# Performance work log

Hardware: AMD Instinct MI355X
Metric: run time of the kernel (lower is better)

## Reference

```python
import jax, jax.numpy as jnp
import numpy as np

N_NODES = 100000
N_EDGES = 1600000
NFEAT, NHID, NCLASS = 128, 64, 40


def setup_inputs() -> dict:
    key = jax.random.key(0)
    k_x, k_e, k_w1, k_b1, k_w2, k_b2 = jax.random.split(key, 6)
    x = jax.random.normal(k_x, (N_NODES, NFEAT), dtype=jnp.float32)
    edge_index = jax.random.randint(k_e, (2, N_EDGES), 0, N_NODES, dtype=jnp.int32)
    # Linear params (torch Linear stores weight as [out, in])
    W1 = jax.random.normal(k_w1, (NHID, NFEAT), dtype=jnp.float32) * 0.05
    b1 = jax.random.normal(k_b1, (NHID,), dtype=jnp.float32) * 0.05
    W2 = jax.random.normal(k_w2, (NCLASS, NHID), dtype=jnp.float32) * 0.05
    b2 = jax.random.normal(k_b2, (NCLASS,), dtype=jnp.float32) * 0.05
    return {"x": x, "W1": W1, "b1": b1, "W2": W2, "b2": b2, "edge_index": edge_index}


def _gcn_layer(x, src, dst, W, b):
    """One GraphConvolution: linear, then degree-normalized gather-scale-scatter-add."""
    n = x.shape[0]
    h = x @ W.T + b  # [N, out]
    # degree computed over row (= src), as in the torch message(); self-loops guarantee deg >= 1
    deg = jax.ops.segment_sum(jnp.ones(src.shape[0], dtype=h.dtype), src, num_segments=n)
    dinv = jax.lax.rsqrt(deg)
    norm = dinv[src] * dinv[dst]  # [E]
    msg = norm[:, None] * h[src]  # gather + scale, [E, out]
    return jax.ops.segment_sum(msg, dst, num_segments=n)  # scatter-add into targets


def reference(x, W1, b1, W2, b2, edge_index):
    n = x.shape[0]
    loops = jnp.arange(n, dtype=edge_index.dtype)
    src = jnp.concatenate([edge_index[0], loops])  # add_self_loops
    dst = jnp.concatenate([edge_index[1], loops])
    h = jax.nn.relu(_gcn_layer(x, src, dst, W1, b1))
    # dropout is identity in eval mode (single-partition: owned_nodes == all nodes,
    # so the distributed halo-exchange / feature-replacement block is a no-op)
    out = _gcn_layer(h, src, dst, W2, b2)
    return jax.nn.log_softmax(out, axis=1)
```

## Files before the change

kernel.cpp:

```cpp
#include <hip/hip_runtime.h>
#include <hip/hip_fp16.h>

#define N_NODES 100000
#define N_EDGES 1600000
#define NFEAT 128
#define NHID 64
#define NCLASS 40
#define SCAN_B 256
#define NTOT (N_NODES + 1)
#define PEMAX (N_EDGES + 16 * N_NODES)

#define BPG 8192
#define NGROUPS 13
#define NCHUNKS 32
#define CHUNK_E (N_EDGES / NCHUNKS)
#define HBINS (NGROUPS * BPG)

#define XROWS 80
#define RPT 20

__global__ __launch_bounds__(256) void hist_kernel(const int* __restrict__ src,
                                                   const int* __restrict__ dst,
                                                   int* __restrict__ deg_src,
                                                   int* __restrict__ hc,
                                                   int* __restrict__ rank) {
    __shared__ int hs[BPG], hd[BPG];
    int g = blockIdx.x, c = blockIdx.y;
    int lo = g * BPG;
    for (int i = threadIdx.x; i < BPG; i += 256) { hs[i] = 0; hd[i] = 0; }
    __syncthreads();
    const int4* s4 = (const int4*)(src + (size_t)c * CHUNK_E);
    const int4* d4 = (const int4*)(dst + (size_t)c * CHUNK_E);
    int n4 = CHUNK_E / 4;
    for (int i = threadIdx.x; i < n4; i += 256) {
        int4 s = s4[i], d = d4[i];
        if ((unsigned)(s.x - lo) < BPG) atomicAdd(&hs[s.x - lo], 1);
        if ((unsigned)(s.y - lo) < BPG) atomicAdd(&hs[s.y - lo], 1);
        if ((unsigned)(s.z - lo) < BPG) atomicAdd(&hs[s.z - lo], 1);
        if ((unsigned)(s.w - lo) < BPG) atomicAdd(&hs[s.w - lo], 1);
        int eb = c * CHUNK_E + 4 * i;
        if ((unsigned)(d.x - lo) < BPG) rank[eb + 0] = atomicAdd(&hd[d.x - lo], 1);
        if ((unsigned)(d.y - lo) < BPG) rank[eb + 1] = atomicAdd(&hd[d.y - lo], 1);
        if ((unsigned)(d.z - lo) < BPG) rank[eb + 2] = atomicAdd(&hd[d.z - lo], 1);
        if ((unsigned)(d.w - lo) < BPG) rank[eb + 3] = atomicAdd(&hd[d.w - lo], 1);
    }
    __syncthreads();
    for (int i = threadIdx.x; i < BPG; i += 256) {
        int v = hs[i];
        if (v) atomicAdd(&deg_src[lo + i], v);
        hc[(size_t)c * HBINS + lo + i] = hd[i];
    }
}

__global__ void dinv_kernel(const int* __restrict__ deg, float* __restrict__ dinv) {
    int i = blockIdx.x * blockDim.x + threadIdx.x;
    if (i < N_NODES) dinv[i] = rsqrtf((float)(deg[i] + 1));
}

__global__ void colsum_kernel(const int* __restrict__ hc, int* __restrict__ pcnt) {
    int b = blockIdx.x * 256 + threadIdx.x;
    if (b >= NTOT) return;
    if (b == N_NODES) { pcnt[b] = 0; return; }
    int s = 0;
    #pragma unroll 8
    for (int c = 0; c < NCHUNKS; ++c) s += hc[(size_t)c * HBINS + b];
    pcnt[b] = (s + 15) & ~15;
}

__global__ void scan1_kernel(const int* __restrict__ cnt, int* __restrict__ partial,
                             int* __restrict__ bsums) {
    __shared__ int tmp[SCAN_B];
    int gid = blockIdx.x * SCAN_B + threadIdx.x;
    int v = (gid < NTOT) ? cnt[gid] : 0;
    tmp[threadIdx.x] = v;
    __syncthreads();
    for (int off = 1; off < SCAN_B; off <<= 1) {
        int t = (threadIdx.x >= off) ? tmp[threadIdx.x - off] : 0;
        __syncthreads();
        tmp[threadIdx.x] += t;
        __syncthreads();
    }
    if (gid < NTOT) partial[gid] = tmp[threadIdx.x] - v;
    if (threadIdx.x == SCAN_B - 1) bsums[blockIdx.x] = tmp[threadIdx.x];
}

__global__ void scan2_kernel(int* __restrict__ bsums, int nb) {
    __shared__ int tmp[512];
    int v = (threadIdx.x < nb) ? bsums[threadIdx.x] : 0;
    tmp[threadIdx.x] = v;
    __syncthreads();
    for (int off = 1; off < 512; off <<= 1) {
        int t = (threadIdx.x >= off) ? tmp[threadIdx.x - off] : 0;
        __syncthreads();
        tmp[threadIdx.x] += t;
        __syncthreads();
    }
    if (threadIdx.x < nb) bsums[threadIdx.x] = tmp[threadIdx.x] - v;
}

__global__ void scan3_kernel(const int* __restrict__ partial, const int* __restrict__ bsums,
                             int* __restrict__ offs) {
    int gid = blockIdx.x * 256 + threadIdx.x;
    if (gid < NTOT) offs[gid] = partial[gid] + bsums[gid >> 8];
}

__global__ void colbase_kernel(const int* __restrict__ hc, const int* __restrict__ offs,
                               int* __restrict__ base) {
    int b = blockIdx.x * 256 + threadIdx.x;
    if (b >= N_NODES) return;
    int r = offs[b];
    #pragma unroll 8
    for (int c = 0; c < NCHUNKS; ++c) {
        base[(size_t)c * HBINS + b] = r;
        r += hc[(size_t)c * HBINS + b];
    }
}

__global__ __launch_bounds__(256) void fill3_kernel(const int* __restrict__ src,
                                                    const int* __restrict__ dst,
                                                    const float* __restrict__ dinv,
                                                    const int* __restrict__ base,
                                                    const int* __restrict__ rank,
                                                    int2* __restrict__ edges) {
    int e = blockIdx.x * 256 + threadIdx.x;
    if (e >= N_EDGES) return;
    int s = src[e], d = dst[e];
    int c = e / CHUNK_E;
    int pos = base[(size_t)c * HBINS + d] + rank[e];
    edges[pos] = make_int2(s, __float_as_int(dinv[s] * dinv[d]));
}

__global__ __launch_bounds__(256) void gemm1_kernel(const float* __restrict__ x,
                                                    const float* __restrict__ W1,
                                                    const float* __restrict__ b1,
                                                    __half* __restrict__ h) {
    __shared__ float xs[XROWS * NFEAT];
    __shared__ float wq[(NFEAT / 4) * NHID * 4];
    int tid = threadIdx.x;
    const float4* w4 = (const float4*)W1;
    for (int j = tid; j < NFEAT * NHID / 4; j += 256) {
        int col = j >> 5, k4 = j & 31;
        int rcol = (col + k4) & 63;
        *(float4*)&wq[(k4 * 64 + rcol) * 4] = w4[j];
    }
    int row0 = blockIdx.x * XROWS;
    const float4* xg = (const float4*)(x + (size_t)row0 * NFEAT);
    float4* xs4 = (float4*)xs;
    #pragma unroll 4
    for (int j = tid; j < XROWS * NFEAT / 4; j += 256) xs4[j] = xg[j];
    __syncthreads();

    int col = tid & 63;
    int rg  = tid >> 6;
    const float* xrow = xs + rg * RPT * NFEAT;
    float acc[RPT];
    #pragma unroll
    for (int r = 0; r < RPT; ++r) acc[r] = 0.f;

    #pragma unroll 2
    for (int k4 = 0; k4 < NFEAT / 4; ++k4) {
        int rcol = (col + k4) & 63;
        float4 w = *(const float4*)&wq[(k4 * 64 + rcol) * 4];
        #pragma unroll
        for (int r = 0; r < RPT; ++r) {
            float4 a = *(const float4*)&xrow[r * NFEAT + k4 * 4];
            acc[r] += a.x * w.x + a.y * w.y + a.z * w.z + a.w * w.w;
        }
    }
    float bb = b1[col];
    #pragma unroll
    for (int r = 0; r < RPT; ++r)
        h[(size_t)(row0 + rg * RPT + r) * NHID + col] = __float2half(acc[r] + bb);
}

__global__ __launch_bounds__(256) void agg1_kernel(const int* __restrict__ offs,
                                                   const float* __restrict__ dinv,
                                                   const int2* __restrict__ edges,
                                                   const __half* __restrict__ h,
                                                   __half* __restrict__ z) {
    int wid = (blockIdx.x * 256 + threadIdx.x) >> 6;
    if (wid >= N_NODES) return;
    int lane = threadIdx.x & 63;
    int hw = lane >> 5;
    int fl = lane & 31;
    int start = offs[wid];
    int myn = (offs[wid + 1] - start) >> 1;
    const int2* eb = edges + start + hw * myn;
    float ax = 0.f, ay = 0.f;
    for (int j = 0; j < myn; j += 8) {
        int2 e0 = eb[j],     e1 = eb[j + 1], e2 = eb[j + 2], e3 = eb[j + 3];
        int2 e4 = eb[j + 4], e5 = eb[j + 5], e6 = eb[j + 6], e7 = eb[j + 7];
        float2 f0 = __half22float2(*(const __half2*)(h + ((size_t)e0.x << 6) + 2 * fl));
        float2 f1 = __half22float2(*(const __half2*)(h + ((size_t)e1.x << 6) + 2 * fl));
        float2 f2 = __half22float2(*(const __half2*)(h + ((size_t)e2.x << 6) + 2 * fl));
        float2 f3 = __half22float2(*(const __half2*)(h + ((size_t)e3.x << 6) + 2 * fl));
        float2 f4 = __half22float2(*(const __half2*)(h + ((size_t)e4.x << 6) + 2 * fl));
        float2 f5 = __half22float2(*(const __half2*)(h + ((size_t)e5.x << 6) + 2 * fl));
        float2 f6 = __half22float2(*(const __half2*)(h + ((size_t)e6.x << 6) + 2 * fl));
        float2 f7 = __half22float2(*(const __half2*)(h + ((size_t)e7.x << 6) + 2 * fl));
        float w0 = __int_as_float(e0.y), w1 = __int_as_float(e1.y);
        float w2 = __int_as_float(e2.y), w3 = __int_as_float(e3.y);
        float w4 = __int_as_float(e4.y), w5 = __int_as_float(e5.y);
        float w6 = __int_as_float(e6.y), w7 = __int_as_float(e7.y);
        ax += w0 * f0.x + w1 * f1.x + w2 * f2.x + w3 * f3.x
            + w4 * f4.x + w5 * f5.x + w6 * f6.x + w7 * f7.x;
        ay += w0 * f0.y + w1 * f1.y + w2 * f2.y + w3 * f3.y
            + w4 * f4.y + w5 * f5.y + w6 * f6.y + w7 * f7.y;
    }
    ax += __shfl_xor(ax, 32);
    ay += __shfl_xor(ay, 32);
    if (hw == 0) {
        float di = dinv[wid];
        float2 f = __half22float2(*(const __half2*)(h + ((size_t)wid << 6) + 2 * fl));
        ax += di * di * f.x;
        ay += di * di * f.y;
        *(__half2*)(z + ((size_t)wid << 6) + 2 * fl) =
            __floats2half2_rn(fmaxf(ax, 0.f), fmaxf(ay, 0.f));
    }
}

__global__ __launch_bounds__(256) void agg2f_kernel(const int* __restrict__ offs,
                                                    const float* __restrict__ dinv,
                                                    const int2* __restrict__ edges,
                                                    const __half* __restrict__ z,
                                                    const float* __restrict__ W2,
                                                    const float* __restrict__ b2,
                                                    float* __restrict__ out) {
    __shared__ float W2l[NHID * NCLASS];
    __shared__ float b2l[NCLASS];
    __shared__ float zs[4 * NHID];
    for (int idx = threadIdx.x; idx < NCLASS * NHID; idx += 256) {
        int c = idx / NHID, k = idx % NHID;
        W2l[k * NCLASS + c] = W2[idx];
    }
    if (threadIdx.x < NCLASS) b2l[threadIdx.x] = b2[threadIdx.x];
    __syncthreads();

    int wid = (blockIdx.x * 256 + threadIdx.x) >> 6;
    if (wid >= N_NODES) return;
    int lane = threadIdx.x & 63;
    int wv = threadIdx.x >> 6;
    int hw = lane >> 5;
    int fl = lane & 31;
    int start = offs[wid];
    int myn = (offs[wid + 1] - start) >> 1;
    const int2* eb = edges + start + hw * myn;
    float ax = 0.f, ay = 0.f, wsum = 0.f;
    for (int j = 0; j < myn; j += 8) {
        int2 e0 = eb[j],     e1 = eb[j + 1], e2 = eb[j + 2], e3 = eb[j + 3];
        int2 e4 = eb[j + 4], e5 = eb[j + 5], e6 = eb[j + 6], e7 = eb[j + 7];
        float2 f0 = __half22float2(*(const __half2*)(z + ((size_t)e0.x << 6) + 2 * fl));
        float2 f1 = __half22float2(*(const __half2*)(z + ((size_t)e1.x << 6) + 2 * fl));
        float2 f2 = __half22float2(*(const __half2*)(z + ((size_t)e2.x << 6) + 2 * fl));
        float2 f3 = __half22float2(*(const __half2*)(z + ((size_t)e3.x << 6) + 2 * fl));
        float2 f4 = __half22float2(*(const __half2*)(z + ((size_t)e4.x << 6) + 2 * fl));
        float2 f5 = __half22float2(*(const __half2*)(z + ((size_t)e5.x << 6) + 2 * fl));
        float2 f6 = __half22float2(*(const __half2*)(z + ((size_t)e6.x << 6) + 2 * fl));
        float2 f7 = __half22float2(*(const __half2*)(z + ((size_t)e7.x << 6) + 2 * fl));
        float w0 = __int_as_float(e0.y), w1 = __int_as_float(e1.y);
        float w2 = __int_as_float(e2.y), w3 = __int_as_float(e3.y);
        float w4 = __int_as_float(e4.y), w5 = __int_as_float(e5.y);
        float w6 = __int_as_float(e6.y), w7 = __int_as_float(e7.y);
        ax += w0 * f0.x + w1 * f1.x + w2 * f2.x + w3 * f3.x
            + w4 * f4.x + w5 * f5.x + w6 * f6.x + w7 * f7.x;
        ay += w0 * f0.y + w1 * f1.y + w2 * f2.y + w3 * f3.y
            + w4 * f4.y + w5 * f5.y + w6 * f6.y + w7 * f7.y;
        wsum += w0 + w1 + w2 + w3 + w4 + w5 + w6 + w7;
    }
    ax += __shfl_xor(ax, 32);
    ay += __shfl_xor(ay, 32);
    wsum += __shfl_xor(wsum, 32);
    float di = dinv[wid];
    float dsq = di * di;
    float2 fz = __half22float2(*(const __half2*)(z + ((size_t)wid << 6) + 2 * fl));
    ax += dsq * fz.x;
    ay += dsq * fz.y;
    wsum += dsq;
    if (hw == 0) *(float2*)&zs[wv * NHID + 2 * fl] = make_float2(ax, ay);
    int c = lane;
    float acc = 0.f;
    if (c < NCLASS) {
        const float* zw = &zs[wv * NHID];
        #pragma unroll 8
        for (int k = 0; k < NHID; ++k) acc += zw[k] * W2l[k * NCLASS + c];
        acc += wsum * b2l[c];
    }
    float m = (c < NCLASS) ? acc : -INFINITY;
    #pragma unroll
    for (int o = 32; o > 0; o >>= 1) m = fmaxf(m, __shfl_xor(m, o));
    float ex = (c < NCLASS) ? __expf(acc - m) : 0.f;
    float s = ex;
    #pragma unroll
    for (int o = 32; o > 0; o >>= 1) s += __shfl_xor(s, o);
    if (c < NCLASS) out[(size_t)wid * NCLASS + c] = acc - m - logf(s);
}

extern "C" void kernel_launch(void* const* d_in, const int* in_sizes, int n_in,
                              void* d_out, int out_size, void* d_ws, size_t ws_size,
                              hipStream_t stream) {
    const float* x  = (const float*)d_in[0];
    const float* W1 = (const float*)d_in[1];
    const float* b1 = (const float*)d_in[2];
    const float* W2 = (const float*)d_in[3];
    const float* b2 = (const float*)d_in[4];
    const int*   ei = (const int*)d_in[5];
    const int* src = ei;
    const int* dst = ei + N_EDGES;
    float* out = (float*)d_out;

    char* ws = (char*)d_ws;
    int*    deg_src = (int*)ws;    ws += 400128;
    int*    pcnt    = (int*)ws;    ws += 400128;
    int*    offs    = (int*)ws;    ws += 400128;
    int*    partial = (int*)ws;    ws += 400128;
    int*    bsums   = (int*)ws;    ws += 2048;
    float*  dinv    = (float*)ws;  ws += 400128;
    int*    hc      = (int*)ws;    ws += (size_t)NCHUNKS * HBINS * sizeof(int);
    int*    base    = (int*)ws;    ws += (size_t)NCHUNKS * HBINS * sizeof(int);
    int*    rank    = (int*)ws;    ws += (size_t)N_EDGES * sizeof(int);
    int2*   edges   = (int2*)ws;   ws += (size_t)PEMAX * sizeof(int2);
    __half* h       = (__half*)ws; ws += (size_t)N_NODES * NHID * sizeof(__half);
    __half* z       = (__half*)ws; ws += (size_t)N_NODES * NHID * sizeof(__half);

    hipMemsetAsync(deg_src, 0, (size_t)N_NODES * sizeof(int), stream);
    hipMemsetAsync(edges, 0, (size_t)PEMAX * sizeof(int2), stream);

    dim3 hgrid(NGROUPS, NCHUNKS);
    hist_kernel<<<hgrid, 256, 0, stream>>>(src, dst, deg_src, hc, rank);
    dinv_kernel<<<(N_NODES + 255) / 256, 256, 0, stream>>>(deg_src, dinv);
    colsum_kernel<<<(NTOT + 255) / 256, 256, 0, stream>>>(hc, pcnt);

    int nsb = (NTOT + SCAN_B - 1) / SCAN_B;
    scan1_kernel<<<nsb, SCAN_B, 0, stream>>>(pcnt, partial, bsums);
    scan2_kernel<<<1, 512, 0, stream>>>(bsums, nsb);
    scan3_kernel<<<(NTOT + 255) / 256, 256, 0, stream>>>(partial, bsums, offs);
    colbase_kernel<<<(N_NODES + 255) / 256, 256, 0, stream>>>(hc, offs, base);

    fill3_kernel<<<(N_EDGES + 255) / 256, 256, 0, stream>>>(src, dst, dinv, base, rank, edges);

    gemm1_kernel<<<N_NODES / XROWS, 256, 0, stream>>>(x, W1, b1, h);

    int nwblk = (N_NODES * 64 + 255) / 256;
    agg1_kernel<<<nwblk, 256, 0, stream>>>(offs, dinv, edges, h, z);
    agg2f_kernel<<<nwblk, 256, 0, stream>>>(offs, dinv, edges, z, W2, b2, out);
}
```

Measured before the change: 294.9 us.

## Apply W2 before second aggregation so gather uses 40-wide features

Splits the fused aggregate-then-project kernel into a separate GEMM (z·W2ᵀ+b2 stored as fp16 in a 64-stride buffer) followed by an aggregation over the 40 projected columns with log_softmax. This reorders linear projection and aggregation so the gather only reads 40 of 64 columns per edge and drops the per-node matvec and weight-sum from the aggregation. It adds an extra kernel launch, an extra intermediate buffer round trip, and extra fp16 rounding of the projected values. Gathered row stride stays 128 bytes, so cache-line traffic per edge may not shrink much.

```diff
diff --git a/kernel.cpp b/kernel.cpp
--- a/kernel.cpp
+++ b/kernel.cpp
@@ -219,80 +219,85 @@
     }
 }
 
-__global__ __launch_bounds__(256) void agg2f_kernel(const int* __restrict__ offs,
-                                                    const float* __restrict__ dinv,
-                                                    const int2* __restrict__ edges,
-                                                    const __half* __restrict__ z,
+__global__ __launch_bounds__(256) void gemm2_kernel(const __half* __restrict__ z,
                                                     const float* __restrict__ W2,
                                                     const float* __restrict__ b2,
-                                                    float* __restrict__ out) {
-    __shared__ float W2l[NHID * NCLASS];
-    __shared__ float b2l[NCLASS];
-    __shared__ float zs[4 * NHID];
+                                                    __half* __restrict__ h2p) {
+    __shared__ float Wl[NHID * NCLASS];
     for (int idx = threadIdx.x; idx < NCLASS * NHID; idx += 256) {
         int c = idx / NHID, k = idx % NHID;
-        W2l[k * NCLASS + c] = W2[idx];
-    }
-    if (threadIdx.x < NCLASS) b2l[threadIdx.x] = b2[threadIdx.x];
-    __syncthreads();
-
+        Wl[k * NCLASS + c] = W2[idx];
+    }
+    __syncthreads();
+    int i = blockIdx.x * 256 + threadIdx.x;
+    if (i >= N_NODES * NCLASS) return;
+    int row = i / NCLASS, col = i - row * NCLASS;
+    const __half2* a = (const __half2*)(z + (size_t)row * NHID);
+    float acc = b2[col];
+    #pragma unroll 8
+    for (int k2 = 0; k2 < NHID / 2; ++k2) {
+        float2 f = __half22float2(a[k2]);
+        acc += f.x * Wl[(2 * k2) * NCLASS + col] + f.y * Wl[(2 * k2 + 1) * NCLASS + col];
+    }
+    h2p[((size_t)row << 6) + col] = __float2half(acc);
+}
+
+__global__ __launch_bounds__(256) void agg2_kernel(const int* __restrict__ offs,
+                                                   const float* __restrict__ dinv,
+                                                   const int2* __restrict__ edges,
+                                                   const __half* __restrict__ h2p,
+                                                   float* __restrict__ out) {
     int wid = (blockIdx.x * 256 + threadIdx.x) >> 6;
     if (wid >= N_NODES) return;
     int lane = threadIdx.x & 63;
-    int wv = threadIdx.x >> 6;
     int hw = lane >> 5;
     int fl = lane & 31;
+    bool act = fl < NCLASS / 2;
     int start = offs[wid];
     int myn = (offs[wid + 1] - start) >> 1;
     const int2* eb = edges + start + hw * myn;
-    float ax = 0.f, ay = 0.f, wsum = 0.f;
-    for (int j = 0; j < myn; j += 8) {
-        int2 e0 = eb[j],     e1 = eb[j + 1], e2 = eb[j + 2], e3 = eb[j + 3];
-        int2 e4 = eb[j + 4], e5 = eb[j + 5], e6 = eb[j + 6], e7 = eb[j + 7];
-        float2 f0 = __half22float2(*(const __half2*)(z + ((size_t)e0.x << 6) + 2 * fl));
-        float2 f1 = __half22float2(*(const __half2*)(z + ((size_t)e1.x << 6) + 2 * fl));
-        float2 f2 = __half22float2(*(const __half2*)(z + ((size_t)e2.x << 6) + 2 * fl));
-        float2 f3 = __half22float2(*(const __half2*)(z + ((size_t)e3.x << 6) + 2 * fl));
-        float2 f4 = __half22float2(*(const __half2*)(z + ((size_t)e4.x << 6) + 2 * fl));
-        float2 f5 = __half22float2(*(const __half2*)(z + ((size_t)e5.x << 6) + 2 * fl));
-        float2 f6 = __half22float2(*(const __half2*)(z + ((size_t)e6.x << 6) + 2 * fl));
-        float2 f7 = __half22float2(*(const __half2*)(z + ((size_t)e7.x << 6) + 2 * fl));
-        float w0 = __int_as_float(e0.y), w1 = __int_as_float(e1.y);
-        float w2 = __int_as_float(e2.y), w3 = __int_as_float(e3.y);
-        float w4 = __int_as_float(e4.y), w5 = __int_as_float(e5.y);
-        float w6 = __int_as_float(e6.y), w7 = __int_as_float(e7.y);
-        ax += w0 * f0.x + w1 * f1.x + w2 * f2.x + w3 * f3.x
-            + w4 * f4.x + w5 * f5.x + w6 * f6.x + w7 * f7.x;
-        ay += w0 * f0.y + w1 * f1.y + w2 * f2.y + w3 * f3.y
-            + w4 * f4.y + w5 * f5.y + w6 * f6.y + w7 * f7.y;
-        wsum += w0 + w1 + w2 + w3 + w4 + w5 + w6 + w7;
+    float ax = 0.f, ay = 0.f;
+    if (act) {
+        for (int j = 0; j < myn; j += 8) {
+            int2 e0 = eb[j],     e1 = eb[j + 1], e2 = eb[j + 2], e3 = eb[j + 3];
+            int2 e4 = eb[j + 4], e5 = eb[j + 5], e6 = eb[j + 6], e7 = eb[j + 7];
+            float2 f0 = __half22float2(*(const __half2*)(h2p + ((size_t)e0.x << 6) + 2 * fl));
+            float2 f1 = __half22float2(*(const __half2*)(h2p + ((size_t)e1.x << 6) + 2 * fl));
+            float2 f2 = __half22float2(*(const __half2*)(h2p + ((size_t)e2.x << 6) + 2 * fl));
+            float2 f3 = __half22float2(*(const __half2*)(h2p + ((size_t)e3.x << 6) + 2 * fl));
+            float2 f4 = __half22float2(*(const __half2*)(h2p + ((size_t)e4.x << 6) + 2 * fl));
+            float2 f5 = __half22float2(*(const __half2*)(h2p + ((size_t)e5.x << 6) + 2 * fl));
+            float2 f6 = __half22float2(*(const __half2*)(h2p + ((size_t)e6.x << 6) + 2 * fl));
+            float2 f7 = __half22float2(*(const __half2*)(h2p + ((size_t)e7.x << 6) + 2 * fl));
+            float w0 = __int_as_float(e0.y), w1 = __int_as_float(e1.y);
+            float w2 = __int_as_float(e2.y), w3 = __int_as_float(e3.y);
+            float w4 = __int_as_float(e4.y), w5 = __int_as_float(e5.y);
+            float w6 = __int_as_float(e6.y), w7 = __int_as_float(e7.y);
+            ax += w0 * f0.x + w1 * f1.x + w2 * f2.x + w3 * f3.x
+                + w4 * f4.x + w5 * f5.x + w6 * f6.x + w7 * f7.x;
+            ay += w0 * f0.y + w1 * f1.y + w2 * f2.y + w3 * f3.y
+                + w4 * f4.y + w5 * f5.y + w6 * f6.y + w7 * f7.y;
+        }
     }
     ax += __shfl_xor(ax, 32);
     ay += __shfl_xor(ay, 32);
-    wsum += __shfl_xor(wsum, 32);
     float di = dinv[wid];
-    float dsq = di * di;
-    float2 fz = __half22float2(*(const __half2*)(z + ((size_t)wid << 6) + 2 * fl));
-    ax += dsq * fz.x;
-    ay += dsq * fz.y;
-    wsum += dsq;
-    if (hw == 0) *(float2*)&zs[wv * NHID + 2 * fl] = make_float2(ax, ay);
-    int c = lane;
-    float acc = 0.f;
-    if (c < NCLASS) {
-        const float* zw = &zs[wv * NHID];
-        #pragma unroll 8
-        for (int k = 0; k < NHID; ++k) acc += zw[k] * W2l[k * NCLASS + c];
-        acc += wsum * b2l[c];
-    }
-    float m = (c < NCLASS) ? acc : -INFINITY;
+    if (act) {
+        float dsq = di * di;
+        float2 f = __half22float2(*(const __half2*)(h2p + ((size_t)wid << 6) + 2 * fl));
+        ax += dsq * f.x;
+        ay += dsq * f.y;
+    }
+    float m = act ? fmaxf(ax, ay) : -INFINITY;
     #pragma unroll
-    for (int o = 32; o > 0; o >>= 1) m = fmaxf(m, __shfl_xor(m, o));
-    float ex = (c < NCLASS) ? __expf(acc - m) : 0.f;
-    float s = ex;
+    for (int o = 16; o > 0; o >>= 1) m = fmaxf(m, __shfl_xor(m, o));
+    float s = act ? (__expf(ax - m) + __expf(ay - m)) : 0.f;
     #pragma unroll
-    for (int o = 32; o > 0; o >>= 1) s += __shfl_xor(s, o);
-    if (c < NCLASS) out[(size_t)wid * NCLASS + c] = acc - m - logf(s);
+    for (int o = 16; o > 0; o >>= 1) s += __shfl_xor(s, o);
+    if (hw == 0 && act) {
+        float lse = m + logf(s);
+        *(float2*)(out + (size_t)wid * NCLASS + 2 * fl) = make_float2(ax - lse, ay - lse);
+    }
 }
 
 extern "C" void kernel_launch(void* const* d_in, const int* in_sizes, int n_in,
@@ -321,6 +326,7 @@
     int2*   edges   = (int2*)ws;   ws += (size_t)PEMAX * sizeof(int2);
     __half* h       = (__half*)ws; ws += (size_t)N_NODES * NHID * sizeof(__half);
     __half* z       = (__half*)ws; ws += (size_t)N_NODES * NHID * sizeof(__half);
+    __half* h2p     = (__half*)ws; ws += (size_t)N_NODES * 64 * sizeof(__half);
 
     hipMemsetAsync(deg_src, 0, (size_t)N_NODES * sizeof(int), stream);
     hipMemsetAsync(edges, 0, (size_t)PEMAX * sizeof(int2), stream);
@@ -342,5 +348,6 @@
 
     int nwblk = (N_NODES * 64 + 255) / 256;
     agg1_kernel<<<nwblk, 256, 0, stream>>>(offs, dinv, edges, h, z);
-    agg2f_kernel<<<nwblk, 256, 0, stream>>>(offs, dinv, edges, z, W2, b2, out);
-}
+    gemm2_kernel<<<(N_NODES * NCLASS + 255) / 256, 256, 0, stream>>>(z, W2, b2, h2p);
+    agg2_kernel<<<nwblk, 256, 0, stream>>>(offs, dinv, edges, h2p, out);
+}
```

Result: faster. 284.0 us (-3.7%).
